# Performance work log

Measured on AMD Instinct MI355X. Metric: run time of the kernel, lower is better.

Reference implementation:

```python
import jax, jax.numpy as jnp
import numpy as np

THRESH = 0.5
RADIUS = 4  # maxpool kernel = 2*RADIUS+1 = 9


def setup_inputs() -> dict:
    key = jax.random.key(0)
    H = W = 8192
    pred_vol = jax.random.uniform(key, (H, W), dtype=jnp.float32)
    return {"pred_vol": pred_vol}


def reference(pred_vol):
    # Faithful translation of Postprocess.forward up through conf_vol
    # (the threshold + 9x9 local-max pooling + equality-compare peak map).
    # The original's torch.nonzero / numpy coordinate extraction is a
    # data-dependent-shape host-side epilogue and is not part of the
    # dense kernel; the dense conf_vol fully determines it.
    k = 2 * RADIUS + 1
    # threshold: keep values strictly above thresh, else 0
    pred_thresh = jnp.where(pred_vol > THRESH, pred_vol, 0.0)
    # local max pool, stride 1, SAME-style padding with -inf (matches
    # torch MaxPool2d implicit -inf padding)
    mp = jax.lax.reduce_window(
        pred_thresh,
        -jnp.inf,
        jax.lax.max,
        window_dimensions=(k, k),
        window_strides=(1, 1),
        padding=((RADIUS, RADIUS), (RADIUS, RADIUS)),
    )
    # keep only positions that are both positive and the local maximum
    conf_vol = jnp.where((mp > 0.0) & (mp == pred_thresh), mp, 0.0)
    return conf_vol
```

## Files before the change

### kernel.cpp

```cpp
#include <hip/hip_runtime.h>


#define W 8192
#define H 8192
#define THRESH 0.5f

typedef float v4f __attribute__((ext_vector_type(4)));

__global__ __launch_bounds__(256, 2) void peak_stream(const float* __restrict__ in,
                                                      float* __restrict__ out) {
    const int lane = threadIdx.x;
    const int col0 = blockIdx.x * 256 + lane * 4;
    const int r0   = (blockIdx.y * 4 + threadIdx.y) * 64;

    const int clc = max(col0 - 4, 0);
    const int crc = min(col0 + 4, W - 4);

    v4f VL[9], VV[9], VR[9];
    v4f hm[9];
    v4f pv[4];

    auto loadrow = [&](int rin, int k) {
        const int rc = min(max(rin, 0), H - 1);
        const float* rowp = in + (size_t)rc * W;
        VL[k] = *(const v4f*)(rowp + clc);
        VV[k] = *(const v4f*)(rowp + col0);
        VR[k] = *(const v4f*)(rowp + crc);
    };

    auto hrow = [&](int k) {
        const v4f l = VL[k], v = VV[k], r = VR[k];
        const float common = fmaxf(fmaxf(fmaxf(l.w, v.x), fmaxf(v.y, v.z)),
                                   fmaxf(v.w, r.x));
        const float m12  = fmaxf(l.y, l.z);
        const float m910 = fmaxf(r.y, r.z);
        v4f o;
        o.x = fmaxf(common, fmaxf(l.x, m12));
        o.y = fmaxf(common, fmaxf(m12, r.y));
        o.z = fmaxf(common, fmaxf(l.z, m910));
        o.w = fmaxf(common, fmaxf(m910, r.w));
        hm[k] = o;
    };

    auto emitrow = [&](int rout, v4f c) {
        v4f m = hm[0];
#pragma unroll
        for (int j = 1; j < 9; ++j) {
            m.x = fmaxf(m.x, hm[j].x);
            m.y = fmaxf(m.y, hm[j].y);
            m.z = fmaxf(m.z, hm[j].z);
            m.w = fmaxf(m.w, hm[j].w);
        }
        v4f ov;
        ov.x = (m.x > THRESH && m.x == c.x) ? m.x : 0.f;
        ov.y = (m.y > THRESH && m.y == c.y) ? m.y : 0.f;
        ov.z = (m.z > THRESH && m.z == c.z) ? m.z : 0.f;
        ov.w = (m.w > THRESH && m.w == c.w) ? m.w : 0.f;
        *(v4f*)(out + (size_t)rout * W + col0) = ov;
    };

#pragma unroll
    for (int k = 0; k < 9; ++k) loadrow(r0 - 4 + k, k);
#pragma unroll
    for (int k = 0; k < 9; ++k) hrow(k);
    emitrow(r0, VV[4]);
#pragma unroll
    for (int j = 0; j < 4; ++j) pv[j] = VV[5 + j];

    for (int c = 1; c < 8; ++c) {
        const int q = r0 - 4 + 9 * c;
#pragma unroll
        for (int k = 0; k < 9; ++k) loadrow(q + k, k);
#pragma unroll
        for (int k = 0; k < 9; ++k) {
            hrow(k);
            emitrow(q + k - 4, (k < 4) ? pv[k] : VV[k - 4]);
        }
#pragma unroll
        for (int j = 0; j < 4; ++j) pv[j] = VV[5 + j];
    }
}

extern "C" void kernel_launch(void* const* d_in, const int* in_sizes, int n_in,
                              void* d_out, int out_size, void* d_ws, size_t ws_size,
                              hipStream_t stream) {
    const float* in = (const float*)d_in[0];
    float* out = (float*)d_out;
    dim3 grid(W / 256, H / 256);
    dim3 block(64, 4, 1);
    peak_stream<<<grid, block, 0, stream>>>(in, out);
}
```

Measured before the change: 441.5 us.

## Fully unroll rolling-window stream with shorter strips and higher occupancy

Replaces the batched 9-row load/compute loop with one fully unrolled 40-step sliding window. Each step loads one row, rotates a 9-entry horizontal-max buffer and a 4-entry center buffer, and emits one output row. Strips shrink from 64 to 32 rows, doubling the grid, and launch bounds ask for 6 blocks per SIMD instead of 2. The goal is lower register pressure and more waves to hide memory latency. The cost is more redundant halo-row reads (8 extra rows per 32 instead of per 64).

```diff
diff --git a/kernel.cpp b/kernel.cpp
--- a/kernel.cpp
+++ b/kernel.cpp
@@ -7,29 +7,28 @@
 
 typedef float v4f __attribute__((ext_vector_type(4)));
 
-__global__ __launch_bounds__(256, 2) void peak_stream(const float* __restrict__ in,
+__global__ __launch_bounds__(256, 6) void peak_stream(const float* __restrict__ in,
                                                       float* __restrict__ out) {
-    const int lane = threadIdx.x;
-    const int col0 = blockIdx.x * 256 + lane * 4;
-    const int r0   = (blockIdx.y * 4 + threadIdx.y) * 64;
+    const int lane  = threadIdx.x;
+    const int col0  = blockIdx.x * 256 + lane * 4;
+    const int strip = blockIdx.y * 4 + threadIdx.y;
+    const int r0    = strip * 32;
 
     const int clc = max(col0 - 4, 0);
     const int crc = min(col0 + 4, W - 4);
 
-    v4f VL[9], VV[9], VR[9];
     v4f hm[9];
-    v4f pv[4];
+    v4f ce[4];
 
-    auto loadrow = [&](int rin, int k) {
-        const int rc = min(max(rin, 0), H - 1);
+#pragma unroll
+    for (int t = 0; t < 40; ++t) {
+        const int rin = r0 - 4 + t;
+        const int rc  = min(max(rin, 0), H - 1);
         const float* rowp = in + (size_t)rc * W;
-        VL[k] = *(const v4f*)(rowp + clc);
-        VV[k] = *(const v4f*)(rowp + col0);
-        VR[k] = *(const v4f*)(rowp + crc);
-    };
+        const v4f l = *(const v4f*)(rowp + clc);
+        const v4f v = *(const v4f*)(rowp + col0);
+        const v4f r = *(const v4f*)(rowp + crc);
 
-    auto hrow = [&](int k) {
-        const v4f l = VL[k], v = VV[k], r = VR[k];
         const float common = fmaxf(fmaxf(fmaxf(l.w, v.x), fmaxf(v.y, v.z)),
                                    fmaxf(v.w, r.x));
         const float m12  = fmaxf(l.y, l.z);
@@ -39,45 +38,28 @@
         o.y = fmaxf(common, fmaxf(m12, r.y));
         o.z = fmaxf(common, fmaxf(l.z, m910));
         o.w = fmaxf(common, fmaxf(m910, r.w));
-        hm[k] = o;
-    };
+        hm[t % 9] = o;
 
-    auto emitrow = [&](int rout, v4f c) {
-        v4f m = hm[0];
+        const v4f cold = ce[t % 4];
+        ce[t % 4] = v;
+
+        if (t >= 8) {
+            v4f m = hm[0];
 #pragma unroll
-        for (int j = 1; j < 9; ++j) {
-            m.x = fmaxf(m.x, hm[j].x);
-            m.y = fmaxf(m.y, hm[j].y);
-            m.z = fmaxf(m.z, hm[j].z);
-            m.w = fmaxf(m.w, hm[j].w);
+            for (int j = 1; j < 9; ++j) {
+                m.x = fmaxf(m.x, hm[j].x);
+                m.y = fmaxf(m.y, hm[j].y);
+                m.z = fmaxf(m.z, hm[j].z);
+                m.w = fmaxf(m.w, hm[j].w);
+            }
+            v4f ov;
+            ov.x = (m.x > THRESH && m.x == cold.x) ? m.x : 0.f;
+            ov.y = (m.y > THRESH && m.y == cold.y) ? m.y : 0.f;
+            ov.z = (m.z > THRESH && m.z == cold.z) ? m.z : 0.f;
+            ov.w = (m.w > THRESH && m.w == cold.w) ? m.w : 0.f;
+            const int rout = rin - 4;
+            *(v4f*)(out + (size_t)rout * W + col0) = ov;
         }
-        v4f ov;
-        ov.x = (m.x > THRESH && m.x == c.x) ? m.x : 0.f;
-        ov.y = (m.y > THRESH && m.y == c.y) ? m.y : 0.f;
-        ov.z = (m.z > THRESH && m.z == c.z) ? m.z : 0.f;
-        ov.w = (m.w > THRESH && m.w == c.w) ? m.w : 0.f;
-        *(v4f*)(out + (size_t)rout * W + col0) = ov;
-    };
-
-#pragma unroll
-    for (int k = 0; k < 9; ++k) loadrow(r0 - 4 + k, k);
-#pragma unroll
-    for (int k = 0; k < 9; ++k) hrow(k);
-    emitrow(r0, VV[4]);
-#pragma unroll
-    for (int j = 0; j < 4; ++j) pv[j] = VV[5 + j];
-
-    for (int c = 1; c < 8; ++c) {
-        const int q = r0 - 4 + 9 * c;
-#pragma unroll
-        for (int k = 0; k < 9; ++k) loadrow(q + k, k);
-#pragma unroll
-        for (int k = 0; k < 9; ++k) {
-            hrow(k);
-            emitrow(q + k - 4, (k < 4) ? pv[k] : VV[k - 4]);
-        }
-#pragma unroll
-        for (int j = 0; j < 4; ++j) pv[j] = VV[5 + j];
     }
 }
 
@@ -86,7 +68,7 @@
                               hipStream_t stream) {
     const float* in = (const float*)d_in[0];
     float* out = (float*)d_out;
-    dim3 grid(W / 256, H / 256);
+    dim3 grid(W / 256, H / 128);
     dim3 block(64, 4, 1);
     peak_stream<<<grid, block, 0, stream>>>(in, out);
 }
```

After: 484.8 us. +9.8%, slower.
